# Kernel tuning notes

Measured on AMD Instinct MI355X. Metric: run time of the kernel, lower is better.

The kernel has to match this reference:

```python
import jax, jax.numpy as jnp
import numpy as np

N_NODES = 100000
N_EDGES = 1600000
N_PAIRS = 200000
IN_C, HID_C, EMB_C, PRED_H = 128, 128, 64, 256


def setup_inputs() -> dict:
    key = jax.random.key(0)
    ks = jax.random.split(key, 12)
    glorot = lambda k, fi, fo: jax.random.normal(k, (fi, fo), jnp.float32) * (2.0 / (fi + fo)) ** 0.5
    return {
        "x": jax.random.normal(ks[0], (N_NODES, IN_C), jnp.float32),
        "edge_index": jax.random.randint(ks[1], (2, N_EDGES), 0, N_NODES, jnp.int64 if jax.config.jax_enable_x64 else jnp.int32),
        "edge_label_index": jax.random.randint(ks[2], (2, N_PAIRS), 0, N_NODES, jnp.int64 if jax.config.jax_enable_x64 else jnp.int32),
        "W1": glorot(ks[3], IN_C, HID_C),
        "b1": jnp.zeros((HID_C,), jnp.float32),
        "W2": glorot(ks[4], HID_C, EMB_C),
        "b2": jnp.zeros((EMB_C,), jnp.float32),
        "Wm1": glorot(ks[5], 4 * EMB_C, PRED_H),
        "bm1": jnp.zeros((PRED_H,), jnp.float32),
        "Wm2": glorot(ks[6], PRED_H, 1),
        "bm2": jnpp if False else jnp.zeros((1,), jnp.float32),
    }


def _gcn_conv(x, W, b, src, dst, n):
    # x: [N, Fin]; src/dst: [E+N] (self-loops included)
    h = x @ W                                              # [N, Fout]
    deg = jax.ops.segment_sum(jnp.ones_like(dst, dtype=h.dtype), dst, num_segments=n)
    dinv = jnp.where(deg > 0, jax.lax.rsqrt(deg), 0.0)     # deg^{-1/2}
    coef = (dinv[src] * dinv[dst])[:, None]                # symmetric norm per edge
    out = jax.ops.segment_sum(h[src] * coef, dst, num_segments=n)
    return out + b


def reference(x, edge_index, edge_label_index, W1, b1, W2, b2, Wm1, bm1, Wm2, bm2):
    n = x.shape[0]
    loop = jnp.arange(n, dtype=edge_index.dtype)
    src = jnp.concatenate([edge_index[0], loop])           # add self-loops (PyG GCNConv default)
    dst = jnp.concatenate([edge_index[1], loop])
    h = jax.nn.relu(_gcn_conv(x, W1, b1, src, dst, n))     # conv1 + relu (dropout p=0/eval)
    z = _gcn_conv(h, W2, b2, src, dst, n)                  # conv2 -> [N, EMB_C]
    zs = z[edge_label_index[0]]                            # [P, EMB_C]
    zd = z[edge_label_index[1]]
    pf = jnp.concatenate([zs, zd, zs * zd, jnp.abs(zs - zd)], axis=-1)  # [P, 4*EMB_C]
    hm = jax.nn.relu(pf @ Wm1 + bm1)
    logits = (hm @ Wm2 + bm2).reshape(-1)                  # [P]
    return logits
```

## Files before the change

### kernel.cpp

```cpp
#include <hip/hip_runtime.h>
#include <hip/hip_bf16.h>
#include <hip/hip_fp16.h>

#define NODES 100000
#define INC 128
#define HIDC 128
#define EMBC 64
#define PREDH 256

#define BSH 9
#define BNODES (1 << BSH)
#define MTILE 8192

typedef __attribute__((ext_vector_type(8))) _Float16 half8;
typedef __attribute__((ext_vector_type(2))) _Float16 half2v;
typedef __attribute__((ext_vector_type(4))) float f32x4;

__global__ void k_deg(const int* __restrict__ ei, int* __restrict__ deg, int E) {
    int e = blockIdx.x * 256 + threadIdx.x;
    if (e >= E) return;
    atomicAdd(&deg[ei[E + e]], 1);
}

__global__ void k_dinv(const int* __restrict__ deg, float* __restrict__ dinv, int n) {
    int i = blockIdx.x * 256 + threadIdx.x;
    if (i >= n) return;
    float c = (float)(deg[i] + 1);
    dinv[i] = 1.0f / sqrtf(c);
}

__global__ __launch_bounds__(1024) void k_scan1(const int* __restrict__ deg,
                                                int* __restrict__ rowptr,
                                                int* __restrict__ bsum, int n) {
    __shared__ int tmp[1024];
    int tid = threadIdx.x;
    int i = blockIdx.x * 1024 + tid;
    int v = (i < n) ? deg[i] : 0;
    tmp[tid] = v;
    __syncthreads();
    for (int off = 1; off < 1024; off <<= 1) {
        int t = (tid >= off) ? tmp[tid - off] : 0;
        __syncthreads();
        tmp[tid] += t;
        __syncthreads();
    }
    if (i < n) rowptr[i] = tmp[tid] - v;
    if (tid == 1023) bsum[blockIdx.x] = tmp[1023];
}

__global__ __launch_bounds__(128) void k_scan2(int* __restrict__ bsum, int nb) {
    __shared__ int tmp[128];
    int tid = threadIdx.x;
    int v = (tid < nb) ? bsum[tid] : 0;
    tmp[tid] = v;
    __syncthreads();
    for (int off = 1; off < 128; off <<= 1) {
        int t = (tid >= off) ? tmp[tid - off] : 0;
        __syncthreads();
        tmp[tid] += t;
        __syncthreads();
    }
    if (tid < nb) bsum[tid] = tmp[tid] - v;
}

__global__ __launch_bounds__(1024) void k_scan3(int* __restrict__ rowptr,
                                                const int* __restrict__ bsum, int n) {
    int i = blockIdx.x * 1024 + threadIdx.x;
    if (i >= n) return;
    rowptr[i] += bsum[blockIdx.x];
}

__global__ void k_bcur(const int* __restrict__ rowptr, int* __restrict__ gcur, int NB) {
    int b = blockIdx.x * 256 + threadIdx.x;
    if (b >= NB) return;
    gcur[b] = rowptr[b << BSH];
}

template <int NB>
__global__ __launch_bounds__(256) void k_msplit(const int* __restrict__ ei,
                                                int* __restrict__ gcur,
                                                unsigned* __restrict__ ebuf, int E) {
    __shared__ int lcnt[NB];
    __shared__ int lbase[NB];
    int tid = threadIdx.x;
    int t0 = blockIdx.x * MTILE;
    int iend = min(t0 + MTILE, E);
    for (int i = tid; i < NB; i += 256) lcnt[i] = 0;
    __syncthreads();
    for (int i = t0 + tid; i < iend; i += 256)
        atomicAdd(&lcnt[ei[E + i] >> BSH], 1);
    __syncthreads();
    for (int i = tid; i < NB; i += 256) {
        int c = lcnt[i];
        lbase[i] = c ? atomicAdd(&gcur[i], c) : 0;
        lcnt[i] = 0;
    }
    __syncthreads();
    for (int i = t0 + tid; i < iend; i += 256) {
        int s = ei[i], d = ei[E + i];
        int b = d >> BSH;
        int r = atomicAdd(&lcnt[b], 1);
        ebuf[lbase[b] + r] = ((unsigned)s << BSH) | (unsigned)(d & (BNODES - 1));
    }
}

__global__ __launch_bounds__(256) void k_csrB(const unsigned* __restrict__ ebuf,
                                              const int* __restrict__ rowptr,
                                              int* __restrict__ col, int n, int E) {
    __shared__ int curs[BNODES];
    int b = blockIdx.x;
    int node0 = b << BSH;
    int tid = threadIdx.x;
    for (int i = tid; i < BNODES; i += 256) {
        int nd = node0 + i;
        curs[i] = (nd < n) ? rowptr[nd] : 0;
    }
    int start = rowptr[node0];
    int end = (node0 + BNODES < n) ? rowptr[node0 + BNODES] : E;
    __syncthreads();
    for (int i = start + tid; i < end; i += 256) {
        unsigned v = ebuf[i];
        int pos = atomicAdd(&curs[v & (unsigned)(BNODES - 1)], 1);
        col[pos] = (int)(v >> BSH);
    }
}

template <int K, int N>
__global__ void k_prept(const float* __restrict__ src, _Float16* __restrict__ dst) {
    int i = blockIdx.x * 256 + threadIdx.x;
    if (i >= K * N) return;
    int nn = i / K, kk = i % K;
    dst[i] = (_Float16)src[kk * N + nn];
}

template <int N, int K, bool XF32>
__global__ __launch_bounds__(256) void k_mmf(const void* __restrict__ Xv,
                                             const _Float16* __restrict__ WT,
                                             const float* __restrict__ dinv,
                                             _Float16* __restrict__ O, int M) {
    int tid = threadIdx.x;
    int wid = tid >> 6, lane = tid & 63;
    int lr = lane & 15, kg = lane >> 4;
    int row0 = blockIdx.x * 64 + wid * 16;
    int arow = min(row0 + lr, M - 1);
    const int NF = N / 16;
    f32x4 acc[NF];
#pragma unroll
    for (int nr = 0; nr < NF; nr++) acc[nr] = (f32x4){0.f, 0.f, 0.f, 0.f};

#pragma unroll
    for (int ks = 0; ks < K / 32; ks++) {
        half8 a;
        if (XF32) {
            const float* Xf = (const float*)Xv + (size_t)arow * K + ks * 32 + kg * 8;
            float4 x0 = *(const float4*)Xf;
            float4 x1 = *(const float4*)(Xf + 4);
            a[0] = (_Float16)x0.x; a[1] = (_Float16)x0.y;
            a[2] = (_Float16)x0.z; a[3] = (_Float16)x0.w;
            a[4] = (_Float16)x1.x; a[5] = (_Float16)x1.y;
            a[6] = (_Float16)x1.z; a[7] = (_Float16)x1.w;
        } else {
            a = *(const half8*)((const _Float16*)Xv + (size_t)arow * K + ks * 32 + kg * 8);
        }
#pragma unroll
        for (int nr = 0; nr < NF; nr++) {
            half8 b = *(const half8*)&WT[(size_t)(nr * 16 + lr) * K + ks * 32 + kg * 8];
            acc[nr] = __builtin_amdgcn_mfma_f32_16x16x32_f16(a, b, acc[nr], 0, 0, 0);
        }
    }

    int orow0 = row0 + kg * 4;
    float dv[4];
#pragma unroll
    for (int r = 0; r < 4; r++) dv[r] = dinv[min(orow0 + r, M - 1)];
#pragma unroll
    for (int nr = 0; nr < NF; nr++)
#pragma unroll
        for (int r = 0; r < 4; r++) {
            int orow = orow0 + r;
            if (orow < M)
                O[(size_t)orow * N + nr * 16 + lr] = (_Float16)(acc[nr][r] * dv[r]);
        }
}

template <int C, bool RELU, typename OT>
__global__ __launch_bounds__(256) void k_gath(const _Float16* __restrict__ Hs,
                                              const float* __restrict__ dinv,
                                              const int* __restrict__ rowptr,
                                              const int* __restrict__ deg,
                                              const int* __restrict__ col,
                                              const float* __restrict__ b,
                                              OT* __restrict__ O, int n) {
    const int TPN = C / 2;
    const int NPB = 256 / TPN;
    int node = blockIdx.x * NPB + threadIdx.x / TPN;
    int lane2 = threadIdx.x % TPN;
    if (node >= n) return;
    int start = rowptr[node];
    int cnt = deg[node];
    float dd = dinv[node];

    half2v hself = *(const half2v*)&Hs[(size_t)node * C + lane2 * 2];
    float ax = (float)hself[0], ay = (float)hself[1];

    for (int base = 0; base < cnt; base += TPN) {
        int m = min(cnt - base, TPN);
        int myc = (lane2 < m) ? col[start + base + lane2] : 0;
        int j = 0;
        for (; j + 1 < m; j += 2) {
            int s0 = __shfl(myc, j, TPN);
            int s1 = __shfl(myc, j + 1, TPN);
            half2v h0 = *(const half2v*)&Hs[(size_t)s0 * C + lane2 * 2];
            half2v h1 = *(const half2v*)&Hs[(size_t)s1 * C + lane2 * 2];
            ax += (float)h0[0] + (float)h1[0];
            ay += (float)h0[1] + (float)h1[1];
        }
        if (j < m) {
            int s0 = __shfl(myc, j, TPN);
            half2v h0 = *(const half2v*)&Hs[(size_t)s0 * C + lane2 * 2];
            ax += (float)h0[0];
            ay += (float)h0[1];
        }
    }

    float2 bb = ((const float2*)b)[lane2];
    float vx = ax * dd + bb.x;
    float vy = ay * dd + bb.y;
    if (RELU) { vx = fmaxf(vx, 0.f); vy = fmaxf(vy, 0.f); }
    if constexpr (sizeof(OT) == 2) {
        half2v o; o[0] = (_Float16)vx; o[1] = (_Float16)vy;
        *(half2v*)&((_Float16*)O)[(size_t)node * C + lane2 * 2] = o;
    } else {
        ((float2*)((float*)O + (size_t)node * C))[lane2] = make_float2(vx, vy);
    }
}

__global__ __launch_bounds__(256) void k_predm(const float* __restrict__ Z,
                                               const int* __restrict__ eli,
                                               const _Float16* __restrict__ WT,
                                               const float* __restrict__ bm1,
                                               const float* __restrict__ Wm2,
                                               const float* __restrict__ bm2,
                                               float* __restrict__ out, int P) {
    __shared__ _Float16 pf[64][264];
    __shared__ float red[4][64];
    int tid = threadIdx.x;
    int p0 = blockIdx.x * 64;

    {
        int pr = tid >> 2, q = tid & 3;
        int pg = p0 + pr;
        int s = 0, d = 0;
        if (pg < P) { s = eli[pg]; d = eli[P + pg]; }
        const float4* zs4 = (const float4*)(Z + (size_t)s * 64 + q * 16);
        const float4* zd4 = (const float4*)(Z + (size_t)d * 64 + q * 16);
#pragma unroll
        for (int j = 0; j < 4; ++j) {
            float4 a = zs4[j], b = zd4[j];
            int c = q * 16 + j * 4;
            pf[pr][c + 0] = (_Float16)a.x;
            pf[pr][c + 1] = (_Float16)a.y;
            pf[pr][c + 2] = (_Float16)a.z;
            pf[pr][c + 3] = (_Float16)a.w;
            pf[pr][64 + c + 0] = (_Float16)b.x;
            pf[pr][64 + c + 1] = (_Float16)b.y;
            pf[pr][64 + c + 2] = (_Float16)b.z;
            pf[pr][64 + c + 3] = (_Float16)b.w;
            pf[pr][128 + c + 0] = (_Float16)(a.x * b.x);
            pf[pr][128 + c + 1] = (_Float16)(a.y * b.y);
            pf[pr][128 + c + 2] = (_Float16)(a.z * b.z);
            pf[pr][128 + c + 3] = (_Float16)(a.w * b.w);
            pf[pr][192 + c + 0] = (_Float16)fabsf(a.x - b.x);
            pf[pr][192 + c + 1] = (_Float16)fabsf(a.y - b.y);
            pf[pr][192 + c + 2] = (_Float16)fabsf(a.z - b.z);
            pf[pr][192 + c + 3] = (_Float16)fabsf(a.w - b.w);
        }
    }
    __syncthreads();

    int wid = tid >> 6, lane = tid & 63;
    int lr = lane & 15, kg = lane >> 4;
    int n0 = wid * 64;

    float wmv[4], bmv[4];
#pragma unroll
    for (int nr = 0; nr < 4; nr++) {
        int nn = n0 + nr * 16 + lr;
        wmv[nr] = Wm2[nn];
        bmv[nr] = bm1[nn];
    }

    f32x4 acc[4][4];
#pragma unroll
    for (int mr = 0; mr < 4; mr++)
#pragma unroll
        for (int nr = 0; nr < 4; nr++) acc[mr][nr] = (f32x4){0.f, 0.f, 0.f, 0.f};

    for (int ks = 0; ks < 8; ks++) {
        half8 a[4], b[4];
#pragma unroll
        for (int mr = 0; mr < 4; mr++)
            a[mr] = *(const half8*)&pf[mr * 16 + lr][ks * 32 + kg * 8];
#pragma unroll
        for (int nr = 0; nr < 4; nr++)
            b[nr] = *(const half8*)&WT[(size_t)(n0 + nr * 16 + lr) * 256 + ks * 32 + kg * 8];
#pragma unroll
        for (int mr = 0; mr < 4; mr++)
#pragma unroll
            for (int nr = 0; nr < 4; nr++)
                acc[mr][nr] = __builtin_amdgcn_mfma_f32_16x16x32_f16(a[mr], b[nr], acc[mr][nr], 0, 0, 0);
    }

#pragma unroll
    for (int mr = 0; mr < 4; mr++) {
#pragma unroll
        for (int reg = 0; reg < 4; reg++) {
            float p = 0.f;
#pragma unroll
            for (int nr = 0; nr < 4; nr++)
                p += fmaxf(acc[mr][nr][reg] + bmv[nr], 0.f) * wmv[nr];
            p += __shfl_xor(p, 1);
            p += __shfl_xor(p, 2);
            p += __shfl_xor(p, 4);
            p += __shfl_xor(p, 8);
            if (lr == 0) red[wid][mr * 16 + kg * 4 + reg] = p;
        }
    }
    __syncthreads();
    if (tid < 64) {
        int pg = p0 + tid;
        if (pg < P)
            out[pg] = red[0][tid] + red[1][tid] + red[2][tid] + red[3][tid] + bm2[0];
    }
}

extern "C" void kernel_launch(void* const* d_in, const int* in_sizes, int n_in,
                              void* d_out, int out_size, void* d_ws, size_t ws_size,
                              hipStream_t stream) {
    const float* x   = (const float*)d_in[0];
    const int*   ei  = (const int*)d_in[1];
    const int*   eli = (const int*)d_in[2];
    const float* W1  = (const float*)d_in[3];
    const float* b1  = (const float*)d_in[4];
    const float* W2  = (const float*)d_in[5];
    const float* b2  = (const float*)d_in[6];
    const float* Wm1 = (const float*)d_in[7];
    const float* bm1 = (const float*)d_in[8];
    const float* Wm2 = (const float*)d_in[9];
    const float* bm2 = (const float*)d_in[10];
    float* out = (float*)d_out;

    const int n = NODES;
    const int E = in_sizes[1] / 2;
    const int P = in_sizes[2] / 2;
    const int NB = (n + BNODES - 1) / BNODES;

    char* ws = (char*)d_ws;
    size_t off = 0;
    auto alloc = [&](size_t bytes) {
        size_t o = off;
        off += (bytes + 255) & ~(size_t)255;
        return o;
    };
    int*      deg    = (int*)(ws + alloc((size_t)n * 4));
    int*      rowptr = (int*)(ws + alloc((size_t)n * 4));
    int*      gcur   = (int*)(ws + alloc(512 * 4));
    unsigned* ebuf   = (unsigned*)(ws + alloc((size_t)E * 4));
    int*      colx   = (int*)(ws + alloc((size_t)E * 4));
    int*      bsum   = (int*)(ws + alloc(512 * 4));
    float*    dinv   = (float*)(ws + alloc((size_t)n * 4));
    _Float16* WmT    = (_Float16*)(ws + alloc((size_t)256 * 256 * 2));
    _Float16* W1T    = (_Float16*)(ws + alloc((size_t)128 * 128 * 2));
    _Float16* W2T    = (_Float16*)(ws + alloc((size_t)64 * 128 * 2));
    _Float16* Hs1    = (_Float16*)(ws + alloc((size_t)n * HIDC * 2));
    _Float16* C1     = (_Float16*)(ws + alloc((size_t)n * HIDC * 2));
    _Float16* Hs2    = (_Float16*)(ws + alloc((size_t)n * EMBC * 2));
    float*    Z      = (float*)(ws + alloc((size_t)n * EMBC * 4));

    hipMemsetAsync(deg, 0, (size_t)n * 4, stream);
    k_deg<<<(E + 255) / 256, 256, 0, stream>>>(ei, deg, E);
    k_prept<256, 256><<<(256 * 256 + 255) / 256, 256, 0, stream>>>(Wm1, WmT);
    k_prept<128, 128><<<(128 * 128 + 255) / 256, 256, 0, stream>>>(W1, W1T);
    k_prept<128, 64><<<(128 * 64 + 255) / 256, 256, 0, stream>>>(W2, W2T);
    int nb = (n + 1023) / 1024;
    k_scan1<<<nb, 1024, 0, stream>>>(deg, rowptr, bsum, n);
    k_scan2<<<1, 128, 0, stream>>>(bsum, nb);
    k_scan3<<<nb, 1024, 0, stream>>>(rowptr, bsum, n);
    k_bcur<<<(NB + 255) / 256, 256, 0, stream>>>(rowptr, gcur, NB);
    k_msplit<196><<<(E + MTILE - 1) / MTILE, 256, 0, stream>>>(ei, gcur, ebuf, E);
    k_csrB<<<NB, 256, 0, stream>>>(ebuf, rowptr, colx, n, E);
    k_dinv<<<(n + 255) / 256, 256, 0, stream>>>(deg, dinv, n);

    int mmGrid = (n + 63) / 64;

    k_mmf<HIDC, INC, true><<<mmGrid, 256, 0, stream>>>(x, W1T, dinv, Hs1, n);
    {
        const int NPB = 256 / (HIDC / 2);
        k_gath<HIDC, true, _Float16><<<(n + NPB - 1) / NPB, 256, 0, stream>>>(
            Hs1, dinv, rowptr, deg, colx, b1, C1, n);
    }

    k_mmf<EMBC, HIDC, false><<<mmGrid, 256, 0, stream>>>(C1, W2T, dinv, Hs2, n);
    {
        const int NPB = 256 / (EMBC / 2);
        k_gath<EMBC, false, float><<<(n + NPB - 1) / NPB, 256, 0, stream>>>(
            Hs2, dinv, rowptr, deg, colx, b2, Z, n);
    }

    k_predm<<<(P + 63) / 64, 256, 0, stream>>>(Z, eli, WmT, bm1, Wm2, bm2, out, P);
}
```

Measured before the change: 469.4 us.

## Vectorize GCN gather with half8 loads, store Z in fp16, merge prep kernels

Rewrites the neighbor gather so each wavefront handles one node, with lanes split into groups that each load a full 16-byte half8 row slice for different edges, then reduces across groups with shuffles. Z is now stored in fp16, which halves its write and the predictor's gather traffic. The three weight transpose kernels are merged into one, and the dinv and gcur computations are folded into the scan kernel to cut launches. Storing Z in fp16 reduces precision, and the per-node wavefront mapping may underuse lanes for low-degree nodes.

```diff
diff --git a/kernel.cpp b/kernel.cpp
--- a/kernel.cpp
+++ b/kernel.cpp
@@ -13,20 +13,12 @@
 #define MTILE 8192
 
 typedef __attribute__((ext_vector_type(8))) _Float16 half8;
-typedef __attribute__((ext_vector_type(2))) _Float16 half2v;
 typedef __attribute__((ext_vector_type(4))) float f32x4;
 
 __global__ void k_deg(const int* __restrict__ ei, int* __restrict__ deg, int E) {
     int e = blockIdx.x * 256 + threadIdx.x;
     if (e >= E) return;
     atomicAdd(&deg[ei[E + e]], 1);
-}
-
-__global__ void k_dinv(const int* __restrict__ deg, float* __restrict__ dinv, int n) {
-    int i = blockIdx.x * 256 + threadIdx.x;
-    if (i >= n) return;
-    float c = (float)(deg[i] + 1);
-    dinv[i] = 1.0f / sqrtf(c);
 }
 
 __global__ __launch_bounds__(1024) void k_scan1(const int* __restrict__ deg,
@@ -64,16 +56,16 @@
 }
 
 __global__ __launch_bounds__(1024) void k_scan3(int* __restrict__ rowptr,
-                                                const int* __restrict__ bsum, int n) {
+                                                const int* __restrict__ bsum,
+                                                const int* __restrict__ deg,
+                                                float* __restrict__ dinv,
+                                                int* __restrict__ gcur, int n) {
     int i = blockIdx.x * 1024 + threadIdx.x;
     if (i >= n) return;
-    rowptr[i] += bsum[blockIdx.x];
-}
-
-__global__ void k_bcur(const int* __restrict__ rowptr, int* __restrict__ gcur, int NB) {
-    int b = blockIdx.x * 256 + threadIdx.x;
-    if (b >= NB) return;
-    gcur[b] = rowptr[b << BSH];
+    int r = rowptr[i] + bsum[blockIdx.x];
+    rowptr[i] = r;
+    dinv[i] = rsqrtf((float)(deg[i] + 1));
+    if ((i & (BNODES - 1)) == 0) gcur[i >> BSH] = r;
 }
 
 template <int NB>
@@ -125,12 +117,22 @@
     }
 }
 
-template <int K, int N>
-__global__ void k_prept(const float* __restrict__ src, _Float16* __restrict__ dst) {
+__global__ void k_prepall(const float* __restrict__ Wm1, const float* __restrict__ W1,
+                          const float* __restrict__ W2, _Float16* __restrict__ WmT,
+                          _Float16* __restrict__ W1T, _Float16* __restrict__ W2T) {
     int i = blockIdx.x * 256 + threadIdx.x;
-    if (i >= K * N) return;
-    int nn = i / K, kk = i % K;
-    dst[i] = (_Float16)src[kk * N + nn];
+    if (i < 256 * 256) {
+        int nn = i >> 8, kk = i & 255;
+        WmT[i] = (_Float16)Wm1[kk * 256 + nn];
+    } else if (i < 256 * 256 + 128 * 128) {
+        int j = i - 256 * 256;
+        int nn = j >> 7, kk = j & 127;
+        W1T[j] = (_Float16)W1[kk * 128 + nn];
+    } else if (i < 256 * 256 + 128 * 128 + 64 * 128) {
+        int j = i - 256 * 256 - 128 * 128;
+        int nn = j >> 7, kk = j & 127;
+        W2T[j] = (_Float16)W2[kk * 64 + nn];
+    }
 }
 
 template <int N, int K, bool XF32>
@@ -183,59 +185,59 @@
         }
 }
 
-template <int C, bool RELU, typename OT>
+template <int C, bool RELU>
 __global__ __launch_bounds__(256) void k_gath(const _Float16* __restrict__ Hs,
                                               const float* __restrict__ dinv,
                                               const int* __restrict__ rowptr,
                                               const int* __restrict__ deg,
                                               const int* __restrict__ col,
                                               const float* __restrict__ b,
-                                              OT* __restrict__ O, int n) {
-    const int TPN = C / 2;
-    const int NPB = 256 / TPN;
-    int node = blockIdx.x * NPB + threadIdx.x / TPN;
-    int lane2 = threadIdx.x % TPN;
+                                              _Float16* __restrict__ O, int n) {
+    const int LPR = C / 8;
+    const int EPI = 64 / LPR;
+    int wid = threadIdx.x >> 6;
+    int node = blockIdx.x * 4 + wid;
     if (node >= n) return;
+    int lane = threadIdx.x & 63;
+    int grp = lane / LPR;
+    int lane2 = lane % LPR;
     int start = rowptr[node];
     int cnt = deg[node];
     float dd = dinv[node];
 
-    half2v hself = *(const half2v*)&Hs[(size_t)node * C + lane2 * 2];
-    float ax = (float)hself[0], ay = (float)hself[1];
-
-    for (int base = 0; base < cnt; base += TPN) {
-        int m = min(cnt - base, TPN);
-        int myc = (lane2 < m) ? col[start + base + lane2] : 0;
-        int j = 0;
-        for (; j + 1 < m; j += 2) {
-            int s0 = __shfl(myc, j, TPN);
-            int s1 = __shfl(myc, j + 1, TPN);
-            half2v h0 = *(const half2v*)&Hs[(size_t)s0 * C + lane2 * 2];
-            half2v h1 = *(const half2v*)&Hs[(size_t)s1 * C + lane2 * 2];
-            ax += (float)h0[0] + (float)h1[0];
-            ay += (float)h0[1] + (float)h1[1];
-        }
-        if (j < m) {
-            int s0 = __shfl(myc, j, TPN);
-            half2v h0 = *(const half2v*)&Hs[(size_t)s0 * C + lane2 * 2];
-            ax += (float)h0[0];
-            ay += (float)h0[1];
-        }
-    }
-
-    float2 bb = ((const float2*)b)[lane2];
-    float vx = ax * dd + bb.x;
-    float vy = ay * dd + bb.y;
-    if (RELU) { vx = fmaxf(vx, 0.f); vy = fmaxf(vy, 0.f); }
-    if constexpr (sizeof(OT) == 2) {
-        half2v o; o[0] = (_Float16)vx; o[1] = (_Float16)vy;
-        *(half2v*)&((_Float16*)O)[(size_t)node * C + lane2 * 2] = o;
-    } else {
-        ((float2*)((float*)O + (size_t)node * C))[lane2] = make_float2(vx, vy);
-    }
-}
-
-__global__ __launch_bounds__(256) void k_predm(const float* __restrict__ Z,
+    float acc[8] = {0.f, 0.f, 0.f, 0.f, 0.f, 0.f, 0.f, 0.f};
+    for (int j = 0; j < cnt; j += EPI) {
+        int e = j + grp;
+        if (e < cnt) {
+            int s = col[start + e];
+            half8 h = *(const half8*)&Hs[(size_t)s * C + lane2 * 8];
+#pragma unroll
+            for (int t = 0; t < 8; t++) acc[t] += (float)h[t];
+        }
+    }
+#pragma unroll
+    for (int t = 0; t < 8; t++) {
+        float v = acc[t];
+#pragma unroll
+        for (int off = LPR; off < 64; off <<= 1)
+            v += __shfl_xor(v, off);
+        acc[t] = v;
+    }
+    if (grp == 0) {
+        half8 hs = *(const half8*)&Hs[(size_t)node * C + lane2 * 8];
+        const float* bp = b + lane2 * 8;
+        half8 o;
+#pragma unroll
+        for (int t = 0; t < 8; t++) {
+            float v = (acc[t] + (float)hs[t]) * dd + bp[t];
+            if (RELU) v = fmaxf(v, 0.f);
+            o[t] = (_Float16)v;
+        }
+        *(half8*)&O[(size_t)node * C + lane2 * 8] = o;
+    }
+}
+
+__global__ __launch_bounds__(256) void k_predm(const _Float16* __restrict__ Z,
                                                const int* __restrict__ eli,
                                                const _Float16* __restrict__ WT,
                                                const float* __restrict__ bm1,
@@ -252,28 +254,20 @@
         int pg = p0 + pr;
         int s = 0, d = 0;
         if (pg < P) { s = eli[pg]; d = eli[P + pg]; }
-        const float4* zs4 = (const float4*)(Z + (size_t)s * 64 + q * 16);
-        const float4* zd4 = (const float4*)(Z + (size_t)d * 64 + q * 16);
-#pragma unroll
-        for (int j = 0; j < 4; ++j) {
-            float4 a = zs4[j], b = zd4[j];
-            int c = q * 16 + j * 4;
-            pf[pr][c + 0] = (_Float16)a.x;
-            pf[pr][c + 1] = (_Float16)a.y;
-            pf[pr][c + 2] = (_Float16)a.z;
-            pf[pr][c + 3] = (_Float16)a.w;
-            pf[pr][64 + c + 0] = (_Float16)b.x;
-            pf[pr][64 + c + 1] = (_Float16)b.y;
-            pf[pr][64 + c + 2] = (_Float16)b.z;
-            pf[pr][64 + c + 3] = (_Float16)b.w;
-            pf[pr][128 + c + 0] = (_Float16)(a.x * b.x);
-            pf[pr][128 + c + 1] = (_Float16)(a.y * b.y);
-            pf[pr][128 + c + 2] = (_Float16)(a.z * b.z);
-            pf[pr][128 + c + 3] = (_Float16)(a.w * b.w);
-            pf[pr][192 + c + 0] = (_Float16)fabsf(a.x - b.x);
-            pf[pr][192 + c + 1] = (_Float16)fabsf(a.y - b.y);
-            pf[pr][192 + c + 2] = (_Float16)fabsf(a.z - b.z);
-            pf[pr][192 + c + 3] = (_Float16)fabsf(a.w - b.w);
+        const half8* zs8 = (const half8*)(Z + (size_t)s * 64 + q * 16);
+        const half8* zd8 = (const half8*)(Z + (size_t)d * 64 + q * 16);
+#pragma unroll
+        for (int h = 0; h < 2; ++h) {
+            half8 za = zs8[h], zb = zd8[h];
+            int c = q * 16 + h * 8;
+#pragma unroll
+            for (int t = 0; t < 8; ++t) {
+                float a = (float)za[t], bb = (float)zb[t];
+                pf[pr][c + t] = za[t];
+                pf[pr][64 + c + t] = zb[t];
+                pf[pr][128 + c + t] = (_Float16)(a * bb);
+                pf[pr][192 + c + t] = (_Float16)fabsf(a - bb);
+            }
         }
     }
     __syncthreads();
@@ -375,37 +369,28 @@
     _Float16* Hs1    = (_Float16*)(ws + alloc((size_t)n * HIDC * 2));
     _Float16* C1     = (_Float16*)(ws + alloc((size_t)n * HIDC * 2));
     _Float16* Hs2    = (_Float16*)(ws + alloc((size_t)n * EMBC * 2));
-    float*    Z      = (float*)(ws + alloc((size_t)n * EMBC * 4));
+    _Float16* Z      = (_Float16*)(ws + alloc((size_t)n * EMBC * 2));
 
     hipMemsetAsync(deg, 0, (size_t)n * 4, stream);
     k_deg<<<(E + 255) / 256, 256, 0, stream>>>(ei, deg, E);
-    k_prept<256, 256><<<(256 * 256 + 255) / 256, 256, 0, stream>>>(Wm1, WmT);
-    k_prept<128, 128><<<(128 * 128 + 255) / 256, 256, 0, stream>>>(W1, W1T);
-    k_prept<128, 64><<<(128 * 64 + 255) / 256, 256, 0, stream>>>(W2, W2T);
+    {
+        int tot = 256 * 256 + 128 * 128 + 64 * 128;
+        k_prepall<<<(tot + 255) / 256, 256, 0, stream>>>(Wm1, W1, W2, WmT, W1T, W2T);
+    }
     int nb = (n + 1023) / 1024;
     k_scan1<<<nb, 1024, 0, stream>>>(deg, rowptr, bsum, n);
     k_scan2<<<1, 128, 0, stream>>>(bsum, nb);
-    k_scan3<<<nb, 1024, 0, stream>>>(rowptr, bsum, n);
-    k_bcur<<<(NB + 255) / 256, 256, 0, stream>>>(rowptr, gcur, NB);
+    k_scan3<<<nb, 1024, 0, stream>>>(rowptr, bsum, deg, dinv, gcur, n);
     k_msplit<196><<<(E + MTILE - 1) / MTILE, 256, 0, stream>>>(ei, gcur, ebuf, E);
     k_csrB<<<NB, 256, 0, stream>>>(ebuf, rowptr, colx, n, E);
-    k_dinv<<<(n + 255) / 256, 256, 0, stream>>>(deg, dinv, n);
 
     int mmGrid = (n + 63) / 64;
 
     k_mmf<HIDC, INC, true><<<mmGrid, 256, 0, stream>>>(x, W1T, dinv, Hs1, n);
-    {
-        const int NPB = 256 / (HIDC / 2);
-        k_gath<HIDC, true, _Float16><<<(n + NPB - 1) / NPB, 256, 0, stream>>>(
-            Hs1, dinv, rowptr, deg, colx, b1, C1, n);
-    }
+    k_gath<HIDC, true><<<(n + 3) / 4, 256, 0, stream>>>(Hs1, dinv, rowptr, deg, colx, b1, C1, n);
 
     k_mmf<EMBC, HIDC, false><<<mmGrid, 256, 0, stream>>>(C1, W2T, dinv, Hs2, n);
-    {
-        const int NPB = 256 / (EMBC / 2);
-        k_gath<EMBC, false, float><<<(n + NPB - 1) / NPB, 256, 0, stream>>>(
-            Hs2, dinv, rowptr, deg, colx, b2, Z, n);
-    }
+    k_gath<EMBC, false><<<(n + 3) / 4, 256, 0, stream>>>(Hs2, dinv, rowptr, deg, colx, b2, Z, n);
 
     k_predm<<<(P + 63) / 64, 256, 0, stream>>>(Z, eli, WmT, bm1, Wm2, bm2, out, P);
 }
```

After: 459.3 us. -2.1%, faster.
